# Optimization experiments

Hardware: AMD Instinct MI355X
Metric: run time of the kernel (lower is better)

The kernel has to match this reference:

```python
import jax, jax.numpy as jnp
import numpy as np


def setup_inputs() -> dict:
    key = jax.random.key(0)
    k1, k2, k3 = jax.random.split(key, 3)
    N, M, D = 8192, 8192, 64
    return {
        "query": jax.random.normal(k1, (N, D), dtype=jnp.float32),
        "key": jax.random.normal(k2, (M, D), dtype=jnp.float32),
        "value": jax.random.normal(k3, (M, D), dtype=jnp.float32),
        "hyper_c": 1,
        "num_of_method": 2,
    }


def reference(query, key, value, hyper_c, num_of_method):
    # num_of_method == 2 (default): cosine-similarity scores scaled by hyper_c.
    # L2-normalize rows (dim=1), matmul, scale, softmax over keys, weight values.
    q_norm = query / jnp.linalg.norm(query, axis=1, keepdims=True)
    k_norm = key / jnp.linalg.norm(key, axis=1, keepdims=True)
    scores = hyper_c * jnp.einsum("nd,md->nm", q_norm, k_norm)  # [N, M]
    p_attn = jax.nn.softmax(scores, axis=-1)
    res_query = jnp.einsum("nm,md->nd", p_attn, value)  # [N, D]
    return (res_query, p_attn)
```

## Files before the change

### kernel.cpp

```cpp
#include <hip/hip_runtime.h>
#include <hip/hip_bf16.h>
#include <cstdint>
#include <cstddef>

#define NQ 8192
#define NK 8192
#define DD 64
#define KSPLIT 4
#define KRANGE (NK / KSPLIT)
#define KTILE 128
#define NT (KRANGE / KTILE)

typedef __bf16 bf16x8 __attribute__((ext_vector_type(8)));
typedef float f32x16 __attribute__((ext_vector_type(16)));
typedef unsigned short u16;
typedef uint32_t u32;

static __device__ __forceinline__ u16 f2bf(float f) {
    union { float f; uint32_t u; } v; v.f = f;
    uint32_t r = (v.u + 0x7fffu + ((v.u >> 16) & 1u)) >> 16;
    return (u16)r;
}

static __device__ __forceinline__ u32 cvtpk(float lo, float hi) {
    u32 r;
    asm("v_cvt_pk_bf16_f32 %0, %1, %2" : "=v"(r) : "v"(lo), "v"(hi));
    return r;
}

#define GLOAD16(g, l)                                                          \
    __builtin_amdgcn_global_load_lds(                                          \
        (__attribute__((address_space(1))) void*)(g),                          \
        (__attribute__((address_space(3))) void*)(l), 16, 0, 0)

__global__ void k_norm(const float* __restrict__ q, const float* __restrict__ k,
                       u16* __restrict__ qn, u16* __restrict__ kn) {
    int wid  = (blockIdx.x * blockDim.x + threadIdx.x) >> 6;
    int lane = threadIdx.x & 63;
    int nw   = (gridDim.x * blockDim.x) >> 6;
    for (int row = wid; row < 2 * NQ; row += nw) {
        const float* src = (row < NQ) ? q : k;
        u16* dst = (row < NQ) ? qn : kn;
        int r = row & (NQ - 1);
        float x = src[(size_t)r * DD + lane];
        float ss = x * x;
        #pragma unroll
        for (int m = 1; m < 64; m <<= 1) ss += __shfl_xor(ss, m, 64);
        dst[(size_t)r * DD + lane] = f2bf(x * rsqrtf(ss));
    }
}

__global__ void k_transv(const float* __restrict__ v, u16* __restrict__ vT) {
    __shared__ float ts[64][65];
    int mb = blockIdx.x * 64;
    int t = threadIdx.x;
    #pragma unroll
    for (int i = 0; i < 16; i++) {
        int idx = i * 256 + t;
        int r = idx >> 6, c = idx & 63;
        ts[r][c] = v[(size_t)(mb + r) * DD + c];
    }
    __syncthreads();
    #pragma unroll
    for (int i = 0; i < 16; i++) {
        int idx = i * 256 + t;
        int d = idx >> 6, m = idx & 63;
        vT[(size_t)d * NK + mb + m] = f2bf(ts[m][d]);
    }
}

__global__ __launch_bounds__(256, 2) void
k_flash(const u16* __restrict__ qn, const u16* __restrict__ kn,
        const u16* __restrict__ vT, const int* __restrict__ hcp,
        float* __restrict__ prs, float* __restrict__ ppv) {
    __shared__ __align__(16) u16 qs[32 * 64];
    __shared__ __align__(16) union SmT {
        struct { u16 ks[128 * 64]; u16 vs[64 * 128]; } t[2];
        struct { float redA[32 * 64]; float redB[32 * 64]; } ep;
    } sm;
    __shared__ float rs_ws[4][32];

    const float hc = (float)hcp[0];
    const int t = threadIdx.x;
    const int w = t >> 6;
    const int lane = t & 63;
    const int l31 = lane & 31;
    const int half = lane >> 5;
    const int qb = (blockIdx.x >> 2) * 32;
    const int sp = blockIdx.x & 3;
    const int k0 = sp * KRANGE;
    const int kw = w * 32;

#define STAGE_KV(B, KB)                                                        \
    do {                                                                       \
        const u16* ksrc_ = kn + (size_t)(k0 + (KB) * KTILE) * DD;              \
        const u16* vsrc_ = vT + (size_t)(k0 + (KB) * KTILE);                   \
        _Pragma("unroll")                                                      \
        for (int i_ = 0; i_ < 4; i_++) {                                       \
            int idx_ = (w * 4 + i_) * 64 + lane;                               \
            int kr_ = idx_ >> 3, kc_ = idx_ & 7;                               \
            GLOAD16(ksrc_ + (size_t)kr_ * DD + ((kc_ ^ (kr_ & 7)) * 8),        \
                    &sm.t[B].ks[(w * 4 + i_) * 512]);                          \
            int vr_ = idx_ >> 4, vc_ = idx_ & 15;                              \
            GLOAD16(vsrc_ + (size_t)vr_ * NK + ((vc_ ^ (vr_ & 7)) * 8),        \
                    &sm.t[B].vs[(w * 4 + i_) * 512]);                          \
        }                                                                      \
    } while (0)

    {
        int row = t >> 3, c = t & 7;
        *reinterpret_cast<uint4*>(&qs[row * 64 + ((c ^ (row & 7)) * 8)]) =
            *reinterpret_cast<const uint4*>(&qn[(size_t)(qb + row) * DD + c * 8]);
    }

    float rs_sum = 0.f;
    f32x16 pv0, pv1;
    #pragma unroll
    for (int i = 0; i < 16; i++) { pv0[i] = 0.f; pv1[i] = 0.f; }

    STAGE_KV(0, 0);
    __syncthreads();

    int cur = 0;
    for (int kb = 0; kb < NT; kb++) {
        if (kb + 1 < NT) STAGE_KV(cur ^ 1, kb + 1);

        const u16* ks_ = sm.t[cur].ks;
        const u16* vs_ = sm.t[cur].vs;

        f32x16 acc;
        #pragma unroll
        for (int i = 0; i < 16; i++) acc[i] = 0.f;
        #pragma unroll
        for (int s = 0; s < 4; s++) {
            int ca = 2 * s + half;
            int kr = kw + l31;
            bf16x8 af = *reinterpret_cast<const bf16x8*>(&ks_[kr * 64 + ((ca ^ (kr & 7)) * 8)]);
            bf16x8 bf = *reinterpret_cast<const bf16x8*>(&qs[l31 * 64 + ((ca ^ (l31 & 7)) * 8)]);
            acc = __builtin_amdgcn_mfma_f32_32x32x16_bf16(af, bf, acc, 0, 0, 0);
        }
        float e[16];
        #pragma unroll
        for (int r = 0; r < 16; r++) {
            e[r] = __expf(acc[r] * hc);
            rs_sum += e[r];
        }
        bf16x8 pa[2];
        #pragma unroll
        for (int s = 0; s < 2; s++) {
            u32 x0 = cvtpk(e[8 * s + 0], e[8 * s + 1]);
            u32 y0 = cvtpk(e[8 * s + 4], e[8 * s + 5]);
            auto r0 = __builtin_amdgcn_permlane32_swap(x0, y0, false, false);
            u32 x1 = cvtpk(e[8 * s + 2], e[8 * s + 3]);
            u32 y1 = cvtpk(e[8 * s + 6], e[8 * s + 7]);
            auto r1 = __builtin_amdgcn_permlane32_swap(x1, y1, false, false);
            union { u32 u[4]; bf16x8 v; } f;
            f.u[0] = r0[0]; f.u[1] = r1[0]; f.u[2] = r0[1]; f.u[3] = r1[1];
            pa[s] = f.v;
        }
        #pragma unroll
        for (int s = 0; s < 2; s++) {
            int cv = (kw >> 3) + 2 * s + half;
            int vr0 = l31, vr1 = 32 + l31;
            bf16x8 b0 = *reinterpret_cast<const bf16x8*>(&vs_[vr0 * 128 + ((cv ^ (vr0 & 7)) * 8)]);
            bf16x8 b1 = *reinterpret_cast<const bf16x8*>(&vs_[vr1 * 128 + ((cv ^ (vr1 & 7)) * 8)]);
            pv0 = __builtin_amdgcn_mfma_f32_32x32x16_bf16(pa[s], b0, pv0, 0, 0, 0);
            pv1 = __builtin_amdgcn_mfma_f32_32x32x16_bf16(pa[s], b1, pv1, 0, 0, 0);
        }

        __syncthreads();
        cur ^= 1;
    }

    rs_sum += __shfl_xor(rs_sum, 32, 64);
    if (lane < 32) rs_ws[w][lane] = rs_sum;
    __syncthreads();
    if (t < 32)
        prs[(size_t)sp * NQ + qb + t] =
            rs_ws[0][t] + rs_ws[1][t] + rs_ws[2][t] + rs_ws[3][t];

    float* redA = sm.ep.redA;
    float* redB = sm.ep.redB;
    if (w == 0) {
        #pragma unroll
        for (int r = 0; r < 16; r++) {
            int qq = (r & 3) + 8 * (r >> 2) + 4 * half;
            redA[qq * 64 + l31] = pv0[r];
            redA[qq * 64 + 32 + l31] = pv1[r];
        }
    } else if (w == 1) {
        #pragma unroll
        for (int r = 0; r < 16; r++) {
            int qq = (r & 3) + 8 * (r >> 2) + 4 * half;
            redB[qq * 64 + l31] = pv0[r];
            redB[qq * 64 + 32 + l31] = pv1[r];
        }
    }
    __syncthreads();
    if (w == 2) {
        #pragma unroll
        for (int r = 0; r < 16; r++) {
            int qq = (r & 3) + 8 * (r >> 2) + 4 * half;
            redA[qq * 64 + l31] += pv0[r];
            redA[qq * 64 + 32 + l31] += pv1[r];
        }
    } else if (w == 3) {
        #pragma unroll
        for (int r = 0; r < 16; r++) {
            int qq = (r & 3) + 8 * (r >> 2) + 4 * half;
            redB[qq * 64 + l31] += pv0[r];
            redB[qq * 64 + 32 + l31] += pv1[r];
        }
    }
    __syncthreads();
    float* dst = ppv + (size_t)sp * NQ * DD + (size_t)qb * DD;
    #pragma unroll
    for (int i = 0; i < 8; i++) {
        int idx = i * 256 + t;
        dst[idx] = redA[idx] + redB[idx];
    }
#undef STAGE_KV
}

__global__ void k_reduce(const float* __restrict__ prs, const float* __restrict__ ppv,
                         float* __restrict__ inv_rs, float* __restrict__ out_res) {
    int id = blockIdx.x * blockDim.x + threadIdx.x;
    int n = id >> 6, d = id & 63;
    float s = prs[n] + prs[NQ + n] + prs[2 * NQ + n] + prs[3 * NQ + n];
    float inv = 1.0f / s;
    if (d == 0) inv_rs[n] = inv;
    const size_t st = (size_t)NQ * DD;
    float v = ppv[id] + ppv[st + id] + ppv[2 * st + id] + ppv[3 * st + id];
    out_res[id] = v * inv;
}

__global__ __launch_bounds__(256, 4) void
k_pwrite(const u16* __restrict__ qn, const u16* __restrict__ kn,
         const float* __restrict__ inv_rs, const int* __restrict__ hcp,
         float* __restrict__ out_p) {
    __shared__ __align__(16) u16 qs2[64 * 64];
    __shared__ __align__(16) u16 ks2[2][64 * 64];

    const float hc = (float)hcp[0];
    const int bid = blockIdx.x;
    const int qb = (bid >> 4) * 64;
    const int kt0 = (bid & 15) * 8;
    const int t = threadIdx.x;
    const int w = t >> 6;
    const int lane = t & 63;
    const int l31 = lane & 31;
    const int half = lane >> 5;
    const int wq = (w >> 1) * 32, wk = (w & 1) * 32;

    #pragma unroll
    for (int i = 0; i < 2; i++) {
        int idx16 = (w * 2 + i) * 64 + lane;
        int row = idx16 >> 3, c = idx16 & 7;
        GLOAD16(qn + (size_t)(qb + row) * DD + ((c ^ (row & 7)) * 8),
                &qs2[(w * 2 + i) * 512]);
    }
#define STAGE_K(B, KT)                                                         \
    do {                                                                       \
        const u16* ksrc_ = kn + (size_t)(KT) * 64 * DD;                        \
        _Pragma("unroll")                                                      \
        for (int i_ = 0; i_ < 2; i_++) {                                       \
            int idx_ = (w * 2 + i_) * 64 + lane;                               \
            int row_ = idx_ >> 3, c_ = idx_ & 7;                               \
            GLOAD16(ksrc_ + (size_t)row_ * DD + ((c_ ^ (row_ & 7)) * 8),       \
                    &ks2[B][(w * 2 + i_) * 512]);                              \
        }                                                                      \
    } while (0)

    STAGE_K(0, kt0);
    const float iv = inv_rs[qb + wq + l31];
    float* rowp = out_p + (size_t)(qb + wq + l31) * NK;
    const int qr = wq + l31;
    __syncthreads();

    int cur = 0;
    for (int i = 0; i < 8; i++) {
        if (i + 1 < 8) STAGE_K(cur ^ 1, kt0 + i + 1);

        f32x16 acc;
        #pragma unroll
        for (int j = 0; j < 16; j++) acc[j] = 0.f;
        #pragma unroll
        for (int s = 0; s < 4; s++) {
            int ca = 2 * s + half;
            int kr = wk + l31;
            bf16x8 a = *reinterpret_cast<const bf16x8*>(&ks2[cur][kr * 64 + ((ca ^ (kr & 7)) * 8)]);
            bf16x8 b = *reinterpret_cast<const bf16x8*>(&qs2[qr * 64 + ((ca ^ (qr & 7)) * 8)]);
            acc = __builtin_amdgcn_mfma_f32_32x32x16_bf16(a, b, acc, 0, 0, 0);
        }
        const int colb = (kt0 + i) * 64 + wk + 4 * half;
        #pragma unroll
        for (int g = 0; g < 4; g++) {
            float4 vv;
            vv.x = __expf(acc[4 * g + 0] * hc) * iv;
            vv.y = __expf(acc[4 * g + 1] * hc) * iv;
            vv.z = __expf(acc[4 * g + 2] * hc) * iv;
            vv.w = __expf(acc[4 * g + 3] * hc) * iv;
            *reinterpret_cast<float4*>(rowp + colb + 8 * g) = vv;
        }
        __syncthreads();
        cur ^= 1;
    }
#undef STAGE_K
}

extern "C" void kernel_launch(void* const* d_in, const int* in_sizes, int n_in,
                              void* d_out, int out_size, void* d_ws, size_t ws_size,
                              hipStream_t stream) {
    const float* q = (const float*)d_in[0];
    const float* k = (const float*)d_in[1];
    const float* v = (const float*)d_in[2];
    const int* hc = (const int*)d_in[3];

    float* out_res = (float*)d_out;
    float* out_p = out_res + (size_t)NQ * DD;

    char* wsb = (char*)d_ws;
    u16* qn = (u16*)wsb;
    u16* kn = qn + (size_t)NQ * DD;
    u16* vT = kn + (size_t)NK * DD;
    float* inv_rs = (float*)(vT + (size_t)NK * DD);

    const size_t base_need = 3 * (size_t)NQ * DD * 2 + (size_t)NQ * 4;
    const size_t extra_need = (size_t)KSPLIT * NQ * 4 + (size_t)KSPLIT * NQ * DD * 4;
    char* extra = (ws_size >= base_need + extra_need)
                      ? wsb + base_need
                      : (char*)out_p + ((size_t)NQ * NK * 4 - extra_need);
    float* prs = (float*)extra;
    float* ppv = prs + (size_t)KSPLIT * NQ;

    k_norm<<<1024, 256, 0, stream>>>(q, k, qn, kn);
    k_transv<<<NK / 64, 256, 0, stream>>>(v, vT);
    k_flash<<<(NQ / 32) * KSPLIT, 256, 0, stream>>>(qn, kn, vT, hc, prs, ppv);
    k_reduce<<<(NQ * DD) / 256, 256, 0, stream>>>(prs, ppv, inv_rs, out_res);
    k_pwrite<<<(NQ / 64) * (NK / 64) / 8, 256, 0, stream>>>(qn, kn, inv_rs, hc, out_p);
}
```

Measured before the change: 377.4 us.

## Pre-pack Q/K/V into MFMA fragment layout and load operands directly from global

The normalize and V-pack kernels now write Q, K and V into a fragment-major layout, so each lane's 8-element bf16 MFMA operand sits in one contiguous 16-byte chunk. The flash and p-write kernels drop LDS staging, double buffering and the barriers, and load operands straight from global memory into registers. LDS use in k_flash shrinks to the epilogue reduction buffers, so launch bounds rise to 3 blocks per CU. The cost is that global-load latency is no longer overlapped by explicit prefetch, and reuse across waves now depends on L1/L2 caching instead of shared memory.

```diff
diff --git a/kernel.cpp b/kernel.cpp
--- a/kernel.cpp
+++ b/kernel.cpp
@@ -16,6 +16,7 @@
 typedef unsigned short u16;
 typedef uint32_t u32;
 
+
 static __device__ __forceinline__ u16 f2bf(float f) {
     union { float f; uint32_t u; } v; v.f = f;
     uint32_t r = (v.u + 0x7fffu + ((v.u >> 16) & 1u)) >> 16;
@@ -28,29 +29,24 @@
     return r;
 }
 
-#define GLOAD16(g, l)                                                          \
-    __builtin_amdgcn_global_load_lds(                                          \
-        (__attribute__((address_space(1))) void*)(g),                          \
-        (__attribute__((address_space(3))) void*)(l), 16, 0, 0)
-
 __global__ void k_norm(const float* __restrict__ q, const float* __restrict__ k,
-                       u16* __restrict__ qn, u16* __restrict__ kn) {
+                       u16* __restrict__ qF, u16* __restrict__ kF) {
     int wid  = (blockIdx.x * blockDim.x + threadIdx.x) >> 6;
     int lane = threadIdx.x & 63;
     int nw   = (gridDim.x * blockDim.x) >> 6;
     for (int row = wid; row < 2 * NQ; row += nw) {
         const float* src = (row < NQ) ? q : k;
-        u16* dst = (row < NQ) ? qn : kn;
+        u16* dst = (row < NQ) ? qF : kF;
         int r = row & (NQ - 1);
         float x = src[(size_t)r * DD + lane];
         float ss = x * x;
         #pragma unroll
         for (int m = 1; m < 64; m <<= 1) ss += __shfl_xor(ss, m, 64);
-        dst[(size_t)r * DD + lane] = f2bf(x * rsqrtf(ss));
-    }
-}
-
-__global__ void k_transv(const float* __restrict__ v, u16* __restrict__ vT) {
+        dst[((size_t)(lane >> 3) * NQ + r) * 8 + (lane & 7)] = f2bf(x * rsqrtf(ss));
+    }
+}
+
+__global__ void k_packv(const float* __restrict__ v, u16* __restrict__ vF) {
     __shared__ float ts[64][65];
     int mb = blockIdx.x * 64;
     int t = threadIdx.x;
@@ -65,19 +61,17 @@
     for (int i = 0; i < 16; i++) {
         int idx = i * 256 + t;
         int d = idx >> 6, m = idx & 63;
-        vT[(size_t)d * NK + mb + m] = f2bf(ts[m][d]);
-    }
-}
-
-__global__ __launch_bounds__(256, 2) void
-k_flash(const u16* __restrict__ qn, const u16* __restrict__ kn,
-        const u16* __restrict__ vT, const int* __restrict__ hcp,
+        int mg = mb + m;
+        vF[((size_t)(mg >> 3) * 64 + d) * 8 + (mg & 7)] = f2bf(ts[m][d]);
+    }
+}
+
+__global__ __launch_bounds__(256, 3) void
+k_flash(const u16* __restrict__ qF, const u16* __restrict__ kF,
+        const u16* __restrict__ vF, const int* __restrict__ hcp,
         float* __restrict__ prs, float* __restrict__ ppv) {
-    __shared__ __align__(16) u16 qs[32 * 64];
-    __shared__ __align__(16) union SmT {
-        struct { u16 ks[128 * 64]; u16 vs[64 * 128]; } t[2];
-        struct { float redA[32 * 64]; float redB[32 * 64]; } ep;
-    } sm;
+    __shared__ float redA[32 * 64];
+    __shared__ float redB[32 * 64];
     __shared__ float rs_ws[4][32];
 
     const float hc = (float)hcp[0];
@@ -91,26 +85,11 @@
     const int k0 = sp * KRANGE;
     const int kw = w * 32;
 
-#define STAGE_KV(B, KB)                                                        \
-    do {                                                                       \
-        const u16* ksrc_ = kn + (size_t)(k0 + (KB) * KTILE) * DD;              \
-        const u16* vsrc_ = vT + (size_t)(k0 + (KB) * KTILE);                   \
-        _Pragma("unroll")                                                      \
-        for (int i_ = 0; i_ < 4; i_++) {                                       \
-            int idx_ = (w * 4 + i_) * 64 + lane;                               \
-            int kr_ = idx_ >> 3, kc_ = idx_ & 7;                               \
-            GLOAD16(ksrc_ + (size_t)kr_ * DD + ((kc_ ^ (kr_ & 7)) * 8),        \
-                    &sm.t[B].ks[(w * 4 + i_) * 512]);                          \
-            int vr_ = idx_ >> 4, vc_ = idx_ & 15;                              \
-            GLOAD16(vsrc_ + (size_t)vr_ * NK + ((vc_ ^ (vr_ & 7)) * 8),        \
-                    &sm.t[B].vs[(w * 4 + i_) * 512]);                          \
-        }                                                                      \
-    } while (0)
-
-    {
-        int row = t >> 3, c = t & 7;
-        *reinterpret_cast<uint4*>(&qs[row * 64 + ((c ^ (row & 7)) * 8)]) =
-            *reinterpret_cast<const uint4*>(&qn[(size_t)(qb + row) * DD + c * 8]);
+    bf16x8 qf[4];
+    #pragma unroll
+    for (int s = 0; s < 4; s++) {
+        int ca = 2 * s + half;
+        qf[s] = *reinterpret_cast<const bf16x8*>(&qF[((size_t)ca * NQ + qb + l31) * 8]);
     }
 
     float rs_sum = 0.f;
@@ -118,27 +97,30 @@
     #pragma unroll
     for (int i = 0; i < 16; i++) { pv0[i] = 0.f; pv1[i] = 0.f; }
 
-    STAGE_KV(0, 0);
-    __syncthreads();
-
-    int cur = 0;
     for (int kb = 0; kb < NT; kb++) {
-        if (kb + 1 < NT) STAGE_KV(cur ^ 1, kb + 1);
-
-        const u16* ks_ = sm.t[cur].ks;
-        const u16* vs_ = sm.t[cur].vs;
-
-        f32x16 acc;
-        #pragma unroll
-        for (int i = 0; i < 16; i++) acc[i] = 0.f;
+        const int kbase = k0 + kb * KTILE;
+
+        bf16x8 af[4], vb0[2], vb1[2];
         #pragma unroll
         for (int s = 0; s < 4; s++) {
             int ca = 2 * s + half;
-            int kr = kw + l31;
-            bf16x8 af = *reinterpret_cast<const bf16x8*>(&ks_[kr * 64 + ((ca ^ (kr & 7)) * 8)]);
-            bf16x8 bf = *reinterpret_cast<const bf16x8*>(&qs[l31 * 64 + ((ca ^ (l31 & 7)) * 8)]);
-            acc = __builtin_amdgcn_mfma_f32_32x32x16_bf16(af, bf, acc, 0, 0, 0);
-        }
+            af[s] = *reinterpret_cast<const bf16x8*>(
+                &kF[((size_t)ca * NK + kbase + kw + l31) * 8]);
+        }
+        #pragma unroll
+        for (int s = 0; s < 2; s++) {
+            int cmg = (kbase >> 3) + (kw >> 3) + 2 * s + half;
+            vb0[s] = *reinterpret_cast<const bf16x8*>(&vF[((size_t)cmg * 64 + l31) * 8]);
+            vb1[s] = *reinterpret_cast<const bf16x8*>(&vF[((size_t)cmg * 64 + 32 + l31) * 8]);
+        }
+
+        f32x16 acc;
+        #pragma unroll
+        for (int i = 0; i < 16; i++) acc[i] = 0.f;
+        #pragma unroll
+        for (int s = 0; s < 4; s++)
+            acc = __builtin_amdgcn_mfma_f32_32x32x16_bf16(af[s], qf[s], acc, 0, 0, 0);
+
         float e[16];
         #pragma unroll
         for (int r = 0; r < 16; r++) {
@@ -160,16 +142,9 @@
         }
         #pragma unroll
         for (int s = 0; s < 2; s++) {
-            int cv = (kw >> 3) + 2 * s + half;
-            int vr0 = l31, vr1 = 32 + l31;
-            bf16x8 b0 = *reinterpret_cast<const bf16x8*>(&vs_[vr0 * 128 + ((cv ^ (vr0 & 7)) * 8)]);
-            bf16x8 b1 = *reinterpret_cast<const bf16x8*>(&vs_[vr1 * 128 + ((cv ^ (vr1 & 7)) * 8)]);
-            pv0 = __builtin_amdgcn_mfma_f32_32x32x16_bf16(pa[s], b0, pv0, 0, 0, 0);
-            pv1 = __builtin_amdgcn_mfma_f32_32x32x16_bf16(pa[s], b1, pv1, 0, 0, 0);
-        }
-
-        __syncthreads();
-        cur ^= 1;
+            pv0 = __builtin_amdgcn_mfma_f32_32x32x16_bf16(pa[s], vb0[s], pv0, 0, 0, 0);
+            pv1 = __builtin_amdgcn_mfma_f32_32x32x16_bf16(pa[s], vb1[s], pv1, 0, 0, 0);
+        }
     }
 
     rs_sum += __shfl_xor(rs_sum, 32, 64);
@@ -179,8 +154,6 @@
         prs[(size_t)sp * NQ + qb + t] =
             rs_ws[0][t] + rs_ws[1][t] + rs_ws[2][t] + rs_ws[3][t];
 
-    float* redA = sm.ep.redA;
-    float* redB = sm.ep.redB;
     if (w == 0) {
         #pragma unroll
         for (int r = 0; r < 16; r++) {
@@ -219,7 +192,6 @@
         int idx = i * 256 + t;
         dst[idx] = redA[idx] + redB[idx];
     }
-#undef STAGE_KV
 }
 
 __global__ void k_reduce(const float* __restrict__ prs, const float* __restrict__ ppv,
@@ -235,12 +207,9 @@
 }
 
 __global__ __launch_bounds__(256, 4) void
-k_pwrite(const u16* __restrict__ qn, const u16* __restrict__ kn,
+k_pwrite(const u16* __restrict__ qF, const u16* __restrict__ kF,
          const float* __restrict__ inv_rs, const int* __restrict__ hcp,
          float* __restrict__ out_p) {
-    __shared__ __align__(16) u16 qs2[64 * 64];
-    __shared__ __align__(16) u16 ks2[2][64 * 64];
-
     const float hc = (float)hcp[0];
     const int bid = blockIdx.x;
     const int qb = (bid >> 4) * 64;
@@ -252,46 +221,31 @@
     const int half = lane >> 5;
     const int wq = (w >> 1) * 32, wk = (w & 1) * 32;
 
-    #pragma unroll
-    for (int i = 0; i < 2; i++) {
-        int idx16 = (w * 2 + i) * 64 + lane;
-        int row = idx16 >> 3, c = idx16 & 7;
-        GLOAD16(qn + (size_t)(qb + row) * DD + ((c ^ (row & 7)) * 8),
-                &qs2[(w * 2 + i) * 512]);
-    }
-#define STAGE_K(B, KT)                                                         \
-    do {                                                                       \
-        const u16* ksrc_ = kn + (size_t)(KT) * 64 * DD;                        \
-        _Pragma("unroll")                                                      \
-        for (int i_ = 0; i_ < 2; i_++) {                                       \
-            int idx_ = (w * 2 + i_) * 64 + lane;                               \
-            int row_ = idx_ >> 3, c_ = idx_ & 7;                               \
-            GLOAD16(ksrc_ + (size_t)row_ * DD + ((c_ ^ (row_ & 7)) * 8),       \
-                    &ks2[B][(w * 2 + i_) * 512]);                              \
-        }                                                                      \
-    } while (0)
-
-    STAGE_K(0, kt0);
-    const float iv = inv_rs[qb + wq + l31];
-    float* rowp = out_p + (size_t)(qb + wq + l31) * NK;
-    const int qr = wq + l31;
-    __syncthreads();
-
-    int cur = 0;
+    const int qr = qb + wq + l31;
+    bf16x8 qf[4];
+    #pragma unroll
+    for (int s = 0; s < 4; s++) {
+        int ca = 2 * s + half;
+        qf[s] = *reinterpret_cast<const bf16x8*>(&qF[((size_t)ca * NQ + qr) * 8]);
+    }
+    const float iv = inv_rs[qr];
+    float* rowp = out_p + (size_t)qr * NK;
+
     for (int i = 0; i < 8; i++) {
-        if (i + 1 < 8) STAGE_K(cur ^ 1, kt0 + i + 1);
-
-        f32x16 acc;
-        #pragma unroll
-        for (int j = 0; j < 16; j++) acc[j] = 0.f;
+        const int krow = (kt0 + i) * 64 + wk + l31;
+        bf16x8 a[4];
         #pragma unroll
         for (int s = 0; s < 4; s++) {
             int ca = 2 * s + half;
-            int kr = wk + l31;
-            bf16x8 a = *reinterpret_cast<const bf16x8*>(&ks2[cur][kr * 64 + ((ca ^ (kr & 7)) * 8)]);
-            bf16x8 b = *reinterpret_cast<const bf16x8*>(&qs2[qr * 64 + ((ca ^ (qr & 7)) * 8)]);
-            acc = __builtin_amdgcn_mfma_f32_32x32x16_bf16(a, b, acc, 0, 0, 0);
-        }
+            a[s] = *reinterpret_cast<const bf16x8*>(&kF[((size_t)ca * NK + krow) * 8]);
+        }
+        f32x16 acc;
+        #pragma unroll
+        for (int j = 0; j < 16; j++) acc[j] = 0.f;
+        #pragma unroll
+        for (int s = 0; s < 4; s++)
+            acc = __builtin_amdgcn_mfma_f32_32x32x16_bf16(a[s], qf[s], acc, 0, 0, 0);
+
         const int colb = (kt0 + i) * 64 + wk + 4 * half;
         #pragma unroll
         for (int g = 0; g < 4; g++) {
@@ -302,10 +256,7 @@
             vv.w = __expf(acc[4 * g + 3] * hc) * iv;
             *reinterpret_cast<float4*>(rowp + colb + 8 * g) = vv;
         }
-        __syncthreads();
-        cur ^= 1;
-    }
-#undef STAGE_K
+    }
 }
 
 extern "C" void kernel_launch(void* const* d_in, const int* in_sizes, int n_in,
@@ -320,10 +271,10 @@
     float* out_p = out_res + (size_t)NQ * DD;
 
     char* wsb = (char*)d_ws;
-    u16* qn = (u16*)wsb;
-    u16* kn = qn + (size_t)NQ * DD;
-    u16* vT = kn + (size_t)NK * DD;
-    float* inv_rs = (float*)(vT + (size_t)NK * DD);
+    u16* qF = (u16*)wsb;
+    u16* kF = qF + (size_t)NQ * DD;
+    u16* vF = kF + (size_t)NK * DD;
+    float* inv_rs = (float*)(vF + (size_t)NK * DD);
 
     const size_t base_need = 3 * (size_t)NQ * DD * 2 + (size_t)NQ * 4;
     const size_t extra_need = (size_t)KSPLIT * NQ * 4 + (size_t)KSPLIT * NQ * DD * 4;
@@ -333,9 +284,9 @@
     float* prs = (float*)extra;
     float* ppv = prs + (size_t)KSPLIT * NQ;
 
-    k_norm<<<1024, 256, 0, stream>>>(q, k, qn, kn);
-    k_transv<<<NK / 64, 256, 0, stream>>>(v, vT);
-    k_flash<<<(NQ / 32) * KSPLIT, 256, 0, stream>>>(qn, kn, vT, hc, prs, ppv);
+    k_norm<<<1024, 256, 0, stream>>>(q, k, qF, kF);
+    k_packv<<<NK / 64, 256, 0, stream>>>(v, vF);
+    k_flash<<<(NQ / 32) * KSPLIT, 256, 0, stream>>>(qF, kF, vF, hc, prs, ppv);
     k_reduce<<<(NQ * DD) / 256, 256, 0, stream>>>(prs, ppv, inv_rs, out_res);
-    k_pwrite<<<(NQ / 64) * (NK / 64) / 8, 256, 0, stream>>>(qn, kn, inv_rs, hc, out_p);
-}
+    k_pwrite<<<(NQ / 64) * (NK / 64) / 8, 256, 0, stream>>>(qF, kF, inv_rs, hc, out_p);
+}
```

Measured after the change: 339.6 us. 1.11x faster.
